# Kernel optimization log

Hardware: AMD Instinct MI355X
Metric: run time of the kernel (lower is better)

Reference implementation:

```python
import jax, jax.numpy as jnp
import numpy as np

B = 8192       # Monte Carlo paths
NSTEP = 30     # Euler time steps
D = 100        # z_dim / number of assets
H1 = 110
H2 = 110
T = NSTEP - 1  # number of subnets
DT = np.float32(1.0 / NSTEP)
R = np.float32(0.05)   # riskfree
EPS = np.float32(1e-3) # Keras BatchNormalization epsilon


def setup_inputs() -> dict:
    key = jax.random.key(0)
    ks = jax.random.split(key, 25)
    f = jnp.float32
    X = jax.random.normal(ks[0], (B, NSTEP, D), f)
    DWs = jax.random.normal(ks[1], (B, NSTEP, D), f) * jnp.sqrt(DT)
    sigmas = jax.random.uniform(ks[2], (D,), f, 0.1, 0.4)
    y_init = jax.random.uniform(ks[3], (1,), f, 0.0, 1.0)
    z_init = jax.random.uniform(ks[4], (1, D), f, -0.1, 0.1)
    W1 = jax.random.normal(ks[5], (T, D, H1), f) / np.sqrt(D).astype(np.float32)
    W2 = jax.random.normal(ks[6], (T, H1, H2), f) / np.sqrt(H1).astype(np.float32)
    W3 = jax.random.normal(ks[7], (T, H2, D), f) / np.sqrt(H2).astype(np.float32)
    dims = [D, H1, H2, D]
    bn = {}
    for j, dim in enumerate(dims):
        bn[f"g{j}"] = 1.0 + 0.1 * jax.random.normal(ks[8 + 4 * j], (T, dim), f)
        bn[f"b{j}"] = 0.05 * jax.random.normal(ks[9 + 4 * j], (T, dim), f)
        bn[f"m{j}"] = 0.1 * jax.random.normal(ks[10 + 4 * j], (T, dim), f)
        bn[f"v{j}"] = jax.random.uniform(ks[11 + 4 * j], (T, dim), f, 0.5, 1.5)
    return dict(X=X, DWs=DWs, sigmas=sigmas, y_init=y_init, z_init=z_init,
                W1=W1, W2=W2, W3=W3, **bn)


def _bn(x, g, b, m, v):
    # Keras BatchNormalization, inference mode
    return (x - m) * jax.lax.rsqrt(v + EPS) * g + b


def _subnet(x, p):
    (w1, w2, w3, g0, b0, m0, v0, g1, b1, m1, v1,
     g2, b2, m2, v2, g3, b3, m3, v3) = p
    x = _bn(x, g0, b0, m0, v0)
    x = jax.nn.relu(x @ w1)
    x = _bn(x, g1, b1, m1, v1)
    x = jax.nn.relu(x @ w2)
    x = _bn(x, g2, b2, m2, v2)
    x = x @ w3
    return _bn(x, g3, b3, m3, v3)


def reference(X, DWs, sigmas, y_init, z_init, W1, W2, W3,
              g0, b0, m0, v0, g1, b1, m1, v1,
              g2, b2, m2, v2, g3, b3, m3, v3):
    nb = X.shape[0]
    Y0 = jnp.ones((nb, 1), X.dtype) * y_init            # [B,1]
    Z0 = jnp.ones((nb, 1), X.dtype) * z_init            # [B,D]

    def step(carry, xs):
        Y, Z = carry
        Xi, Xn, DWi, p = xs
        Y = Y + R * Y * DT + jnp.sum(sigmas * Xi * Z * DWi, axis=1, keepdims=True)
        Z = _subnet(Xn, p)
        return (Y, Z), None

    params = (W1, W2, W3, g0, b0, m0, v0, g1, b1, m1, v1,
              g2, b2, m2, v2, g3, b3, m3, v3)  # each leading dim T
    xs = (jnp.moveaxis(X[:, :T], 1, 0),        # [T,B,D]
          jnp.moveaxis(X[:, 1:T + 1], 1, 0),   # [T,B,D]
          jnp.moveaxis(DWs[:, :T], 1, 0),      # [T,B,D]
          params)
    (Y, Z), _ = jax.lax.scan(step, (Y0, Z0), xs)
    # final step: X[:,-2,:] with DWs[:,-1,:]
    Y = Y + R * Y * DT + jnp.sum(sigmas * X[:, -2, :] * Z * DWs[:, -1, :],
                                 axis=1, keepdims=True)
    return Y
```

## Files before the change

### kernel.cpp

```cpp
#include <hip/hip_runtime.h>

typedef unsigned short ushort_t;
typedef __attribute__((ext_vector_type(8))) short s16x8;
typedef __attribute__((ext_vector_type(4))) float f32x4;

#define B_PATHS 8192
#define NSTEP   30
#define DD      100
#define HH      110
#define TT      29
#define ROWSTR  3000
#define LDK     136
#define WFRAGSZ 14336
#define DT_C    (1.0f/30.0f)
#define R_C     0.05f
#define EPS_C   1e-3f

__device__ __forceinline__ ushort_t f2bf(float f) {
  unsigned u = __float_as_uint(f);
  u = u + 0x7FFFu + ((u >> 16) & 1u);
  return (ushort_t)(u >> 16);
}
__device__ __forceinline__ float bf2f(ushort_t u) {
  return __uint_as_float(((unsigned)u) << 16);
}

__global__ void prep_kernel(const float* __restrict__ W1, const float* __restrict__ W2,
                            const float* __restrict__ W3,
                            const float* g0, const float* b0, const float* m0, const float* v0,
                            const float* g1, const float* b1, const float* m1, const float* v1,
                            const float* g2, const float* b2, const float* m2, const float* v2,
                            const float* g3, const float* b3, const float* m3, const float* v3,
                            ushort_t* __restrict__ wprep, float* __restrict__ bprep)
{
  const int mat = blockIdx.x, t = blockIdx.y, tid = threadIdx.x;
  __shared__ float wsh[110*110];
  __shared__ float sin_[112], hin_[112], sout_[112], hout_[112];

  int Kr, Nr; const float* W; const float *g, *bb, *mm, *vv;
  if (mat == 0)      { Kr = 100; Nr = 110; W = W1 + t*11000; g = g0+t*100; bb = b0+t*100; mm = m0+t*100; vv = v0+t*100; }
  else if (mat == 1) { Kr = 110; Nr = 110; W = W2 + t*12100; g = g1+t*110; bb = b1+t*110; mm = m1+t*110; vv = v1+t*110; }
  else               { Kr = 110; Nr = 100; W = W3 + t*11000; g = g2+t*110; bb = b2+t*110; mm = m2+t*110; vv = v2+t*110; }

  if (tid < Kr) {
    float s = g[tid] * rsqrtf(vv[tid] + EPS_C);
    sin_[tid] = s; hin_[tid] = bb[tid] - mm[tid]*s;
  }
  if (mat == 2 && tid < Nr) {
    float s = g3[t*100+tid] * rsqrtf(v3[t*100+tid] + EPS_C);
    sout_[tid] = s; hout_[tid] = b3[t*100+tid] - m3[t*100+tid]*s;
  }
  for (int i = tid; i < Kr*Nr; i += 256) wsh[i] = W[i];
  __syncthreads();

  if (tid < 128) {
    float c = 0.f;
    if (tid < Nr) {
      for (int k = 0; k < Kr; ++k) c += hin_[k] * wsh[k*Nr + tid];
      if (mat == 2) c = c * sout_[tid] + hout_[tid];
    }
    bprep[(t*3 + mat)*128 + tid] = c;
  }

  ushort_t* wo = wprep + (size_t)(t*3 + mat) * WFRAGSZ;
  for (int ch = tid; ch < 1792; ch += 256) {
    const int lane = ch & 63, ntkb = ch >> 6;
    const int nt = ntkb % 7, kb = ntkb / 7;
    const int n  = nt*16 + (lane & 15);
    const int k0 = kb*32 + (lane >> 4)*8;
    ushort_t tmp[8];
#pragma unroll
    for (int j = 0; j < 8; ++j) {
      const int k = k0 + j;
      float v = 0.f;
      if (n < Nr && k < Kr) {
        v = sin_[k] * wsh[k*Nr + n];
        if (mat == 2) v *= sout_[n];
      }
      tmp[j] = f2bf(v);
    }
    ushort4 lo; lo.x = tmp[0]; lo.y = tmp[1]; lo.z = tmp[2]; lo.w = tmp[3];
    ushort4 hi; hi.x = tmp[4]; hi.y = tmp[5]; hi.z = tmp[6]; hi.w = tmp[7];
    *(ushort4*)(wo + ch*8)     = lo;
    *(ushort4*)(wo + ch*8 + 4) = hi;
  }
}

__device__ __forceinline__ void mlp_stage32(ushort_t* act, const ushort_t* __restrict__ wfrag,
                                            const float* __restrict__ biasg,
                                            int lane, int lrow, int quad, bool relu)
{
  s16x8 aL[4], aH[4];
#pragma unroll
  for (int kb = 0; kb < 4; ++kb) {
    aL[kb] = *(const s16x8*)(act + lrow*LDK + kb*32 + quad*8);
    aH[kb] = *(const s16x8*)(act + (16 + lrow)*LDK + kb*32 + quad*8);
  }
  f32x4 accL[7], accH[7];
  const f32x4 z4 = {0.f, 0.f, 0.f, 0.f};
#pragma unroll
  for (int nt = 0; nt < 7; ++nt) { accL[nt] = z4; accH[nt] = z4; }
#pragma unroll
  for (int kb = 0; kb < 4; ++kb) {
#pragma unroll
    for (int nt = 0; nt < 7; ++nt) {
      s16x8 b = *(const s16x8*)(wfrag + ((kb*7 + nt)*64 + lane)*8);
      accL[nt] = __builtin_amdgcn_mfma_f32_16x16x32_bf16(aL[kb], b, accL[nt], 0, 0, 0);
      accH[nt] = __builtin_amdgcn_mfma_f32_16x16x32_bf16(aH[kb], b, accH[nt], 0, 0, 0);
    }
  }
  __asm__ volatile("" ::: "memory");
#pragma unroll
  for (int nt = 0; nt < 7; ++nt) {
    const int col = nt*16 + lrow;
    const float bv = biasg[col];
#pragma unroll
    for (int r = 0; r < 4; ++r) {
      float uL = accL[nt][r] + bv;
      float uH = accH[nt][r] + bv;
      if (relu) { uL = uL > 0.f ? uL : 0.f; uH = uH > 0.f ? uH : 0.f; }
      act[(quad*4 + r)*LDK + col]        = f2bf(uL);
      act[(16 + quad*4 + r)*LDK + col]   = f2bf(uH);
    }
  }
#pragma unroll
  for (int r = 0; r < 4; ++r) {
    act[(quad*4 + r)*LDK + 112 + lrow]      = 0;
    act[(16 + quad*4 + r)*LDK + 112 + lrow] = 0;
  }
  __asm__ volatile("" ::: "memory");
}

__global__ __launch_bounds__(256, 3)
void subnet_kernel(const float* __restrict__ X, const float* __restrict__ DW,
                   const float* __restrict__ sigmas,
                   const ushort_t* __restrict__ wprep, const float* __restrict__ bprep,
                   float* __restrict__ sbuf)
{
  __shared__ __align__(16) ushort_t act[4][32*LDK];

  const int tid  = threadIdx.x;
  const int wv   = tid >> 6;
  const int t    = blockIdx.y;
  const int m0   = blockIdx.x * 128 + wv * 32;
  const int lane = tid & 63, lrow = lane & 15, quad = lane >> 4;
  const int row2 = lane >> 1, part2 = lane & 1;
  const int brow = m0 + row2;

  ushort_t* A = act[wv];

  const float* xrp = X + (size_t)brow*ROWSTR + (t+1)*DD;
#pragma unroll
  for (int g = 0; g < 16; ++g) {
    const int c = part2 + g*2;
    ushort4 u; u.x = 0; u.y = 0; u.z = 0; u.w = 0;
    if (c < 25) {
      const float4 v = *(const float4*)(xrp + c*4);
      u.x = f2bf(v.x); u.y = f2bf(v.y); u.z = f2bf(v.z); u.w = f2bf(v.w);
    }
    *(ushort4*)(A + row2*LDK + c*4) = u;
  }
  __asm__ volatile("" ::: "memory");

  const ushort_t* wf = wprep + (size_t)(t*3) * WFRAGSZ;
  const float*    bg = bprep + (t*3) * 128;

  mlp_stage32(A, wf,             bg,       lane, lrow, quad, true);
  mlp_stage32(A, wf + WFRAGSZ,   bg + 128, lane, lrow, quad, true);
  mlp_stage32(A, wf + 2*WFRAGSZ, bg + 256, lane, lrow, quad, false);

  {
    const int xt = (t == TT - 1) ? (NSTEP - 2) : (t + 1);
    const float* xe = X  + (size_t)brow*ROWSTR + xt*DD;
    const float* dr = DW + (size_t)brow*ROWSTR + (t+1)*DD;
    float p = 0.f;
#pragma unroll
    for (int g = 0; g < 13; ++g) {
      const int c = part2 + g*2;
      if (c < 25) {
        const float4 xv = *(const float4*)(xe + c*4);
        const float4 dv = *(const float4*)(dr + c*4);
        const float4 sg = *(const float4*)(sigmas + c*4);
        const ushort4 zu = *(const ushort4*)(A + row2*LDK + c*4);
        p += sg.x*xv.x*dv.x*bf2f(zu.x);
        p += sg.y*xv.y*dv.y*bf2f(zu.y);
        p += sg.z*xv.z*dv.z*bf2f(zu.z);
        p += sg.w*xv.w*dv.w*bf2f(zu.w);
      }
    }
    p += __shfl_xor(p, 1, 64);
    if (part2 == 0)
      sbuf[(size_t)(t+1)*B_PATHS + brow] = p;
  }
}

__global__ void y_kernel(const float* __restrict__ X, const float* __restrict__ DW,
                         const float* __restrict__ sigmas, const float* __restrict__ y_init,
                         const float* __restrict__ z_init, const float* __restrict__ sbuf,
                         float* __restrict__ out)
{
  const int b = blockIdx.x * blockDim.x + threadIdx.x;
  const float* xr = X + (size_t)b * ROWSTR;
  const float* dr = DW + (size_t)b * ROWSTR;
  float s0 = 0.f;
#pragma unroll 5
  for (int c = 0; c < 25; ++c) {
    float4 xv = *(const float4*)(xr + c*4);
    float4 dv = *(const float4*)(dr + c*4);
    float4 sg = *(const float4*)(sigmas + c*4);
    float4 zv = *(const float4*)(z_init + c*4);
    s0 += sg.x*xv.x*zv.x*dv.x;
    s0 += sg.y*xv.y*zv.y*dv.y;
    s0 += sg.z*xv.z*zv.z*dv.z;
    s0 += sg.w*xv.w*zv.w*dv.w;
  }
  float y = y_init[0];
  y = y + R_C*y*DT_C + s0;
#pragma unroll
  for (int tau = 1; tau < NSTEP; ++tau)
    y = y + R_C*y*DT_C + sbuf[(size_t)tau*B_PATHS + b];
  out[b] = y;
}

extern "C" void kernel_launch(void* const* d_in, const int* in_sizes, int n_in,
                              void* d_out, int out_size, void* d_ws, size_t ws_size,
                              hipStream_t stream) {
  const float* X      = (const float*)d_in[0];
  const float* DWs    = (const float*)d_in[1];
  const float* sigmas = (const float*)d_in[2];
  const float* y_init = (const float*)d_in[3];
  const float* z_init = (const float*)d_in[4];
  const float* W1     = (const float*)d_in[5];
  const float* W2     = (const float*)d_in[6];
  const float* W3     = (const float*)d_in[7];
  const float* bn[16];
  for (int i = 0; i < 16; ++i) bn[i] = (const float*)d_in[8 + i];

  char* ws = (char*)d_ws;
  ushort_t* wprep = (ushort_t*)ws;
  float*    bprep = (float*)(ws + 2494464);
  float*    sbuf  = (float*)(ws + 2539008);
  float*    out   = (float*)d_out;

  prep_kernel<<<dim3(3, TT), 256, 0, stream>>>(
      W1, W2, W3,
      bn[0], bn[1], bn[2], bn[3],  bn[4], bn[5], bn[6], bn[7],
      bn[8], bn[9], bn[10], bn[11], bn[12], bn[13], bn[14], bn[15],
      wprep, bprep);
  subnet_kernel<<<dim3(B_PATHS/128, TT), 256, 0, stream>>>(
      X, DWs, sigmas, wprep, bprep, sbuf);
  y_kernel<<<dim3(B_PATHS/256), 256, 0, stream>>>(
      X, DWs, sigmas, y_init, z_init, sbuf, out);
}
```

Measured before the change: 349.5 us.

## Chunk time steps per block and pre-weight Y recurrence contributions by growth factor

Each block now loops over a chunk of four time steps instead of handling one, and uses 128-thread blocks with separate input and output activation buffers. Because the Y recurrence is linear, each step's contribution is scaled by the growth factor raised to the number of remaining steps. Contributions are summed per chunk into a small partial buffer, and y_kernel adds eight partials instead of reading 29 rows. The X values used for the next step's dot product come from the bf16 copy already staged in shared memory, so X is read once from global memory but with reduced precision in that term. The change also alters grid shape and occupancy, and the sum order differs from the sequential recurrence.

New measurement: 387.9 us. 11.0% more time.

```diff
diff --git a/kernel.cpp b/kernel.cpp
--- a/kernel.cpp
+++ b/kernel.cpp
@@ -7,13 +7,15 @@
 #define B_PATHS 8192
 #define NSTEP   30
 #define DD      100
-#define HH      110
 #define TT      29
 #define ROWSTR  3000
 #define LDK     136
 #define WFRAGSZ 14336
+#define NCHUNK  8
+#define CHSZ    4
 #define DT_C    (1.0f/30.0f)
 #define R_C     0.05f
+#define GFAC    (1.0f + R_C*DT_C)
 #define EPS_C   1e-3f
 
 __device__ __forceinline__ ushort_t f2bf(float f) {
@@ -86,15 +88,16 @@
   }
 }
 
-__device__ __forceinline__ void mlp_stage32(ushort_t* act, const ushort_t* __restrict__ wfrag,
+__device__ __forceinline__ void mlp_stage32(const ushort_t* actIn, ushort_t* actOut,
+                                            const ushort_t* __restrict__ wfrag,
                                             const float* __restrict__ biasg,
                                             int lane, int lrow, int quad, bool relu)
 {
   s16x8 aL[4], aH[4];
 #pragma unroll
   for (int kb = 0; kb < 4; ++kb) {
-    aL[kb] = *(const s16x8*)(act + lrow*LDK + kb*32 + quad*8);
-    aH[kb] = *(const s16x8*)(act + (16 + lrow)*LDK + kb*32 + quad*8);
+    aL[kb] = *(const s16x8*)(actIn + lrow*LDK + kb*32 + quad*8);
+    aH[kb] = *(const s16x8*)(actIn + (16 + lrow)*LDK + kb*32 + quad*8);
   }
   f32x4 accL[7], accH[7];
   const f32x4 z4 = {0.f, 0.f, 0.f, 0.f};
@@ -119,84 +122,119 @@
       float uL = accL[nt][r] + bv;
       float uH = accH[nt][r] + bv;
       if (relu) { uL = uL > 0.f ? uL : 0.f; uH = uH > 0.f ? uH : 0.f; }
-      act[(quad*4 + r)*LDK + col]        = f2bf(uL);
-      act[(16 + quad*4 + r)*LDK + col]   = f2bf(uH);
+      actOut[(quad*4 + r)*LDK + col]      = f2bf(uL);
+      actOut[(16 + quad*4 + r)*LDK + col] = f2bf(uH);
     }
   }
 #pragma unroll
   for (int r = 0; r < 4; ++r) {
-    act[(quad*4 + r)*LDK + 112 + lrow]      = 0;
-    act[(16 + quad*4 + r)*LDK + 112 + lrow] = 0;
+    actOut[(quad*4 + r)*LDK + 112 + lrow]      = 0;
+    actOut[(16 + quad*4 + r)*LDK + 112 + lrow] = 0;
   }
   __asm__ volatile("" ::: "memory");
 }
 
-__global__ __launch_bounds__(256, 3)
+__global__ __launch_bounds__(128, 2)
 void subnet_kernel(const float* __restrict__ X, const float* __restrict__ DW,
                    const float* __restrict__ sigmas,
                    const ushort_t* __restrict__ wprep, const float* __restrict__ bprep,
-                   float* __restrict__ sbuf)
-{
-  __shared__ __align__(16) ushort_t act[4][32*LDK];
+                   float* __restrict__ pbuf)
+{
+  __shared__ __align__(16) ushort_t actA[2][32*LDK];
+  __shared__ __align__(16) ushort_t actB[2][32*LDK];
 
   const int tid  = threadIdx.x;
   const int wv   = tid >> 6;
-  const int t    = blockIdx.y;
-  const int m0   = blockIdx.x * 128 + wv * 32;
   const int lane = tid & 63, lrow = lane & 15, quad = lane >> 4;
   const int row2 = lane >> 1, part2 = lane & 1;
+  const int m0   = blockIdx.x * 64 + wv * 32;
   const int brow = m0 + row2;
-
-  ushort_t* A = act[wv];
-
-  const float* xrp = X + (size_t)brow*ROWSTR + (t+1)*DD;
-#pragma unroll
-  for (int g = 0; g < 16; ++g) {
-    const int c = part2 + g*2;
-    ushort4 u; u.x = 0; u.y = 0; u.z = 0; u.w = 0;
-    if (c < 25) {
-      const float4 v = *(const float4*)(xrp + c*4);
-      u.x = f2bf(v.x); u.y = f2bf(v.y); u.z = f2bf(v.z); u.w = f2bf(v.w);
-    }
-    *(ushort4*)(A + row2*LDK + c*4) = u;
+  const int c    = blockIdx.y;
+  const int t0   = c * CHSZ, t1 = (t0 + CHSZ < TT) ? t0 + CHSZ : TT;
+
+  ushort_t* A = actA[wv];
+  ushort_t* B = actB[wv];
+
+#pragma unroll
+  for (int g = part2; g < 7; g += 2) {
+    ushort4 z; z.x = 0; z.y = 0; z.z = 0; z.w = 0;
+    *(ushort4*)(A + row2*LDK + (25 + g)*4) = z;
   }
   __asm__ volatile("" ::: "memory");
 
-  const ushort_t* wf = wprep + (size_t)(t*3) * WFRAGSZ;
-  const float*    bg = bprep + (t*3) * 128;
-
-  mlp_stage32(A, wf,             bg,       lane, lrow, quad, true);
-  mlp_stage32(A, wf + WFRAGSZ,   bg + 128, lane, lrow, quad, true);
-  mlp_stage32(A, wf + 2*WFRAGSZ, bg + 256, lane, lrow, quad, false);
-
-  {
-    const int xt = (t == TT - 1) ? (NSTEP - 2) : (t + 1);
-    const float* xe = X  + (size_t)brow*ROWSTR + xt*DD;
+  float P = 0.f;
+
+  for (int t = t0; t < t1; ++t) {
+    const float* xr = X  + (size_t)brow*ROWSTR + (t+1)*DD;
     const float* dr = DW + (size_t)brow*ROWSTR + (t+1)*DD;
+    float4 dwv[13];
+#pragma unroll
+    for (int g = 0; g < 13; ++g) {
+      const int cgrp = part2*13 + g;
+      const int cc   = cgrp < 25 ? cgrp : 24;
+      const float4 xv = *(const float4*)(xr + cc*4);
+      dwv[g] = *(const float4*)(dr + cc*4);
+      if (cgrp < 25) {
+        ushort4 u;
+        u.x = f2bf(xv.x); u.y = f2bf(xv.y); u.z = f2bf(xv.z); u.w = f2bf(xv.w);
+        *(ushort4*)(A + row2*LDK + cgrp*4) = u;
+      }
+    }
+    __asm__ volatile("" ::: "memory");
+
+    const ushort_t* wf = wprep + (size_t)(t*3) * WFRAGSZ;
+    const float*    bg = bprep + (t*3) * 128;
+
+    mlp_stage32(A, B, wf,             bg,       lane, lrow, quad, true);
+    mlp_stage32(B, B, wf + WFRAGSZ,   bg + 128, lane, lrow, quad, true);
+    mlp_stage32(B, B, wf + 2*WFRAGSZ, bg + 256, lane, lrow, quad, false);
+
     float p = 0.f;
-#pragma unroll
-    for (int g = 0; g < 13; ++g) {
-      const int c = part2 + g*2;
-      if (c < 25) {
-        const float4 xv = *(const float4*)(xe + c*4);
-        const float4 dv = *(const float4*)(dr + c*4);
-        const float4 sg = *(const float4*)(sigmas + c*4);
-        const ushort4 zu = *(const ushort4*)(A + row2*LDK + c*4);
-        p += sg.x*xv.x*dv.x*bf2f(zu.x);
-        p += sg.y*xv.y*dv.y*bf2f(zu.y);
-        p += sg.z*xv.z*dv.z*bf2f(zu.z);
-        p += sg.w*xv.w*dv.w*bf2f(zu.w);
+    if (t < TT - 1) {
+#pragma unroll
+      for (int g = 0; g < 13; ++g) {
+        const int cgrp = part2*13 + g;
+        if (cgrp < 25) {
+          const float4 sg = *(const float4*)(sigmas + cgrp*4);
+          const ushort4 xu = *(const ushort4*)(A + row2*LDK + cgrp*4);
+          const ushort4 zu = *(const ushort4*)(B + row2*LDK + cgrp*4);
+          p += sg.x*bf2f(xu.x)*dwv[g].x*bf2f(zu.x);
+          p += sg.y*bf2f(xu.y)*dwv[g].y*bf2f(zu.y);
+          p += sg.z*bf2f(xu.z)*dwv[g].z*bf2f(zu.z);
+          p += sg.w*bf2f(xu.w)*dwv[g].w*bf2f(zu.w);
+        }
+      }
+    } else {
+      const float* xe = X + (size_t)brow*ROWSTR + 28*DD;
+#pragma unroll
+      for (int g = 0; g < 13; ++g) {
+        const int cgrp = part2*13 + g;
+        if (cgrp < 25) {
+          const float4 sg = *(const float4*)(sigmas + cgrp*4);
+          const float4 xv = *(const float4*)(xe + cgrp*4);
+          const ushort4 zu = *(const ushort4*)(B + row2*LDK + cgrp*4);
+          p += sg.x*xv.x*dwv[g].x*bf2f(zu.x);
+          p += sg.y*xv.y*dwv[g].y*bf2f(zu.y);
+          p += sg.z*xv.z*dwv[g].z*bf2f(zu.z);
+          p += sg.w*xv.w*dwv[g].w*bf2f(zu.w);
+        }
       }
     }
     p += __shfl_xor(p, 1, 64);
-    if (part2 == 0)
-      sbuf[(size_t)(t+1)*B_PATHS + brow] = p;
-  }
+
+    float w = 1.f;
+    for (int k = 0; k < 28 - t; ++k) w *= GFAC;
+    P += w * p;
+    __asm__ volatile("" ::: "memory");
+  }
+
+  if (part2 == 0)
+    pbuf[(size_t)c*B_PATHS + brow] = P;
 }
 
 __global__ void y_kernel(const float* __restrict__ X, const float* __restrict__ DW,
                          const float* __restrict__ sigmas, const float* __restrict__ y_init,
-                         const float* __restrict__ z_init, const float* __restrict__ sbuf,
+                         const float* __restrict__ z_init, const float* __restrict__ pbuf,
                          float* __restrict__ out)
 {
   const int b = blockIdx.x * blockDim.x + threadIdx.x;
@@ -214,12 +252,14 @@
     s0 += sg.z*xv.z*zv.z*dv.z;
     s0 += sg.w*xv.w*zv.w*dv.w;
   }
-  float y = y_init[0];
-  y = y + R_C*y*DT_C + s0;
-#pragma unroll
-  for (int tau = 1; tau < NSTEP; ++tau)
-    y = y + R_C*y*DT_C + sbuf[(size_t)tau*B_PATHS + b];
-  out[b] = y;
+  float acc = 0.f;
+#pragma unroll
+  for (int c = 0; c < NCHUNK; ++c) acc += pbuf[(size_t)c*B_PATHS + b];
+
+  float y = y_init[0]*GFAC + s0;
+#pragma unroll
+  for (int k = 0; k < 29; ++k) y *= GFAC;
+  out[b] = y + acc;
 }
 
 extern "C" void kernel_launch(void* const* d_in, const int* in_sizes, int n_in,
@@ -239,7 +279,7 @@
   char* ws = (char*)d_ws;
   ushort_t* wprep = (ushort_t*)ws;
   float*    bprep = (float*)(ws + 2494464);
-  float*    sbuf  = (float*)(ws + 2539008);
+  float*    pbuf  = (float*)(ws + 2539008);
   float*    out   = (float*)d_out;
 
   prep_kernel<<<dim3(3, TT), 256, 0, stream>>>(
@@ -247,8 +287,8 @@
       bn[0], bn[1], bn[2], bn[3],  bn[4], bn[5], bn[6], bn[7],
       bn[8], bn[9], bn[10], bn[11], bn[12], bn[13], bn[14], bn[15],
       wprep, bprep);
-  subnet_kernel<<<dim3(B_PATHS/128, TT), 256, 0, stream>>>(
-      X, DWs, sigmas, wprep, bprep, sbuf);
+  subnet_kernel<<<dim3(B_PATHS/64, NCHUNK), 128, 0, stream>>>(
+      X, DWs, sigmas, wprep, bprep, pbuf);
   y_kernel<<<dim3(B_PATHS/256), 256, 0, stream>>>(
-      X, DWs, sigmas, y_init, z_init, sbuf, out);
-}
+      X, DWs, sigmas, y_init, z_init, pbuf, out);
+}
```
